# Performance work log

Hardware: AMD Instinct MI355X
Metric: run time of the kernel (lower is better)

Reference implementation:

```python
import jax, jax.numpy as jnp
import numpy as np

N, E, D = 50000, 800000, 128      # nodes, edges, input feature dim
H, HEADS, C = 128, 8, 64          # hidden units, attention heads, classes
HEAD_DIM = H // HEADS
NEG_SLOPE = 0.2


def segment_softmax(scores, seg, num_segments):
    # scores: [E, heads]; softmax over edges sharing the same destination node
    m = jax.ops.segment_max(scores, seg, num_segments=num_segments)
    ex = jnp.exp(scores - m[seg])
    s = jax.ops.segment_sum(ex, seg, num_segments=num_segments)
    return ex / (s[seg] + 1e-9)


def gcn_layer(x, src, dst, W, b):
    # mean-aggregate neighbor features along edges, then linear transform
    agg = jax.ops.segment_sum(x[src], dst, num_segments=N)          # [N, d]
    deg = jax.ops.segment_sum(jnp.ones((E,), x.dtype), dst, num_segments=N)
    agg = agg / jnp.maximum(deg, 1.0)[:, None]
    return agg @ W + b


def gat_layer(x, src, dst, Wg, a_src, a_dst, bg):
    h = (x @ Wg).reshape(N, HEADS, HEAD_DIM)                        # [N, heads, hd]
    e_s = jnp.einsum('nhd,hd->nh', h, a_src)                        # [N, heads]
    e_d = jnp.einsum('nhd,hd->nh', h, a_dst)
    scores = jax.nn.leaky_relu(e_s[src] + e_d[dst], NEG_SLOPE)      # [E, heads]
    alpha = segment_softmax(scores, dst, N)                         # [E, heads]
    msg = h[src] * alpha[:, :, None]                                # [E, heads, hd]
    out = jax.ops.segment_sum(msg, dst, num_segments=N).reshape(N, H)
    return out + bg


def setup_inputs() -> dict:
    key = jax.random.key(0)
    ks = jax.random.split(key, 12)
    s = lambda fan: 1.0 / np.sqrt(fan)
    return {
        'node_features': jax.random.normal(ks[0], (N, D), jnp.float32),
        'edge_index': jax.random.randint(ks[1], (2, E), 0, N, jnp.int32),
        'W1': jax.random.normal(ks[2], (D, H), jnp.float32) * s(D),
        'b1': jnp.zeros((H,), jnp.float32),
        'W2': jax.random.normal(ks[3], (H, H), jnp.float32) * s(H),
        'b2': jnp.zeros((H,), jnp.float32),
        'Wg': jax.random.normal(ks[4], (D, H), jnp.float32) * s(D),
        'bg': jnp.zeros((H,), jnp.float32),
        'a_src': jax.random.normal(ks[5], (HEADS, HEAD_DIM), jnp.float32) * s(HEAD_DIM),
        'a_dst': jax.random.normal(ks[6], (HEADS, HEAD_DIM), jnp.float32) * s(HEAD_DIM),
        'Wcls': jax.random.normal(ks[7], (H, C), jnp.float32) * s(H),
        'bcls': jnp.zeros((C,), jnp.float32),
        'Wl': jax.random.normal(ks[8], (H, 1), jnp.float32) * s(H),
        'bl': jnp.zeros((1,), jnp.float32),
    }


def reference(node_features, edge_index, W1, b1, W2, b2, Wg, bg, a_src, a_dst, Wcls, bcls, Wl, bl):
    src, dst = edge_index[0], edge_index[1]
    x = jax.nn.relu(gcn_layer(node_features, src, dst, W1, b1))
    x = jax.nn.relu(gcn_layer(x, src, dst, W2, b2))
    node_classification_output = jax.nn.softmax(x @ Wcls + bcls, axis=-1)  # [N, C]
    x_gat = jax.nn.relu(gat_layer(node_features, src, dst, Wg, a_src, a_dst, bg))
    link_prediction_output = jax.nn.sigmoid(x_gat @ Wl + bl)               # [N, 1]
    return (node_classification_output, link_prediction_output)
```

## Files before the change

### kernel.cpp

```cpp
#include <hip/hip_runtime.h>
#include <math.h>

#define DIM      128
#define HEADS    8
#define NCLS     64
#define NEG_SLOPE 0.2f
#define NPB32    32
#define NPB64    64
#define APAD     132
#define KT       32
#define CAP      48

typedef unsigned int uint32;

__device__ __forceinline__ uint32 pack_bf162(float a, float b) {
    uint32 ua = __float_as_uint(a); ua += 0x7fffu + ((ua >> 16) & 1u);
    uint32 ub = __float_as_uint(b); ub += 0x7fffu + ((ub >> 16) & 1u);
    return (ua >> 16) | (ub & 0xffff0000u);
}
__device__ __forceinline__ float2 unpack_bf162(uint32 u) {
    return make_float2(__uint_as_float(u << 16), __uint_as_float(u & 0xffff0000u));
}

__global__ __launch_bounds__(256, 4)
void proj1_fill(const float* __restrict__ x, const float* __restrict__ Wg,
                const float* __restrict__ a_src, const float* __restrict__ a_dst,
                uint32* __restrict__ zb, float* __restrict__ e_s,
                float* __restrict__ e_d, int N,
                const int* __restrict__ src, const int* __restrict__ dst,
                int* __restrict__ cursor, unsigned short* __restrict__ ell,
                int E, int nProj) {
    __shared__ float A[NPB64 * APAD];
    int tid = threadIdx.x;
    int bid = blockIdx.x;
    int p = bid / 5;
    bool isProj = ((bid % 5) == 0) && (p < nProj);

    if (!isProj) {
        int projBefore = min((bid + 4) / 5, nProj);
        int e = (bid - projBefore) * 256 + tid;
        if (e < E) {
            int d = dst[e];
            int pos = atomicAdd(&cursor[d], 1);
            if (pos < CAP) ell[(size_t)d * CAP + pos] = (unsigned short)src[e];
        }
        return;
    }

    int n0 = p * NPB64;
    for (int idx = tid; idx < NPB64 * 32; idx += 256) {
        int nl = idx >> 5, qq = idx & 31;
        int n = n0 + nl;
        float4 v = (n < N) ? ((const float4*)x)[(size_t)n * 32 + qq]
                           : make_float4(0.f, 0.f, 0.f, 0.f);
        *(float4*)&A[nl * APAD + qq * 4] = v;
    }
    __syncthreads();

    for (int idx = tid; idx < NPB64 * 16; idx += 256) {
        int nl = idx >> 4, u4 = idx & 15;
        int n = n0 + nl;
        if (n < N) {
            float4 va = *(float4*)&A[nl * APAD + u4 * 8];
            float4 vb = *(float4*)&A[nl * APAD + u4 * 8 + 4];
            uint4 o;
            o.x = pack_bf162(va.x, va.y); o.y = pack_bf162(va.z, va.w);
            o.z = pack_bf162(vb.x, vb.y); o.w = pack_bf162(vb.z, vb.w);
            *(uint4*)(zb + (size_t)n * 128 + u4 * 4) = o;
        }
    }

    int fg = tid & 15, ng = tid >> 4;
    int nb = ng * 4;
    const float* W = Wg + (size_t)fg * 8;
    float acc[4][8];
#pragma unroll
    for (int r = 0; r < 4; ++r)
#pragma unroll
        for (int c = 0; c < 8; ++c) acc[r][c] = 0.f;

#pragma unroll 4
    for (int k = 0; k < DIM; ++k) {
        float wv[8];
        *(float4*)&wv[0] = *(const float4*)(W + (size_t)k * DIM);
        *(float4*)&wv[4] = *(const float4*)(W + (size_t)k * DIM + 4);
#pragma unroll
        for (int r = 0; r < 4; ++r) {
            float a = A[(nb + r) * APAD + k];
#pragma unroll
            for (int c = 0; c < 8; ++c) acc[r][c] = fmaf(a, wv[c], acc[r][c]);
        }
    }
#pragma unroll
    for (int r = 0; r < 4; ++r) {
        int n = n0 + nb + r;
        if (n < N) {
            uint32 o[4];
#pragma unroll
            for (int c = 0; c < 4; ++c) o[c] = pack_bf162(acc[r][2 * c], acc[r][2 * c + 1]);
            *(uint4*)(zb + (size_t)n * 128 + 64 + fg * 4) = *(uint4*)o;
        }
    }
    int head = fg >> 1, sub = (fg & 1) * 8;
    float as[8], ad[8];
#pragma unroll
    for (int j = 0; j < 8; ++j) {
        as[j] = a_src[head * 16 + sub + j];
        ad[j] = a_dst[head * 16 + sub + j];
    }
#pragma unroll
    for (int r = 0; r < 4; ++r) {
        int n = n0 + nb + r;
        float ps = 0.f, pd = 0.f;
#pragma unroll
        for (int c = 0; c < 8; ++c) {
            ps = fmaf(acc[r][c], as[c], ps);
            pd = fmaf(acc[r][c], ad[c], pd);
        }
        ps += __shfl_xor(ps, 1);
        pd += __shfl_xor(pd, 1);
        if (n < N && !(fg & 1)) {
            e_s[n * HEADS + head] = ps;
            e_d[n * HEADS + head] = pd;
        }
    }
}

__global__ __launch_bounds__(256, 8)
void mega1(const uint32* __restrict__ zb, const int* __restrict__ cursor,
           const unsigned short* __restrict__ ell, const float* __restrict__ e_s,
           const float* __restrict__ e_d, const float* __restrict__ bg,
           const float* __restrict__ Wl, const float* __restrict__ bl,
           uint32* __restrict__ mxb, float* __restrict__ out_link, int N) {
    int wave = threadIdx.x >> 6, lane = threadIdx.x & 63;
    int n = blockIdx.x * 4 + wave;
    if (n >= N) return;
    int eoff = lane >> 5, q = lane & 31;
    bool isH = q >= 16;
    int head = (max(q, 16) - 16) >> 1;
    float edl = e_d[n * HEADS + head];
    const uint4* zrow = (const uint4*)zb;
    size_t base = (size_t)n * CAP;
    int len = min(cursor[n], CAP);
    float acc[8];
#pragma unroll
    for (int j = 0; j < 8; ++j) acc[j] = 0.f;
    float den = 0.f;
    int it = 0;
    for (; it + 8 <= len; it += 8) {
        int s[4];
#pragma unroll
        for (int k = 0; k < 4; ++k) s[k] = ell[base + it + 2 * k + eoff];
        float es[4]; uint4 u[4];
#pragma unroll
        for (int k = 0; k < 4; ++k) {
            es[k] = e_s[s[k] * HEADS + head];
            u[k]  = zrow[(size_t)s[k] * 32 + q];
        }
#pragma unroll
        for (int k = 0; k < 4; ++k) {
            float sc = es[k] + edl;
            sc = (sc > 0.f) ? sc : NEG_SLOPE * sc;
            float ex = __expf(sc);
            den += ex;
            float w = isH ? ex : 1.f;
            float2 v0 = unpack_bf162(u[k].x), v1 = unpack_bf162(u[k].y);
            float2 v2 = unpack_bf162(u[k].z), v3 = unpack_bf162(u[k].w);
            acc[0] = fmaf(v0.x, w, acc[0]); acc[1] = fmaf(v0.y, w, acc[1]);
            acc[2] = fmaf(v1.x, w, acc[2]); acc[3] = fmaf(v1.y, w, acc[3]);
            acc[4] = fmaf(v2.x, w, acc[4]); acc[5] = fmaf(v2.y, w, acc[5]);
            acc[6] = fmaf(v3.x, w, acc[6]); acc[7] = fmaf(v3.y, w, acc[7]);
        }
    }
    for (; it < len; it += 2) {
        int e = it + eoff;
        bool valid = e < len;
        int s = ell[base + (valid ? e : it)];
        float sc = e_s[s * HEADS + head] + edl;
        sc = (sc > 0.f) ? sc : NEG_SLOPE * sc;
        float ex = __expf(sc);
        uint4 u = zrow[(size_t)s * 32 + q];
        den += valid ? ex : 0.f;
        float w = valid ? (isH ? ex : 1.f) : 0.f;
        float2 v0 = unpack_bf162(u.x), v1 = unpack_bf162(u.y);
        float2 v2 = unpack_bf162(u.z), v3 = unpack_bf162(u.w);
        acc[0] = fmaf(v0.x, w, acc[0]); acc[1] = fmaf(v0.y, w, acc[1]);
        acc[2] = fmaf(v1.x, w, acc[2]); acc[3] = fmaf(v1.y, w, acc[3]);
        acc[4] = fmaf(v2.x, w, acc[4]); acc[5] = fmaf(v2.y, w, acc[5]);
        acc[6] = fmaf(v3.x, w, acc[6]); acc[7] = fmaf(v3.y, w, acc[7]);
    }
#pragma unroll
    for (int j = 0; j < 8; ++j) acc[j] += __shfl_xor(acc[j], 32);
    den += __shfl_xor(den, 32);

    if (!isH && eoff == 0) {
        float inv = 1.f / fmaxf((float)len, 1.f);
        uint4 o;
        o.x = pack_bf162(acc[0] * inv, acc[1] * inv);
        o.y = pack_bf162(acc[2] * inv, acc[3] * inv);
        o.z = pack_bf162(acc[4] * inv, acc[5] * inv);
        o.w = pack_bf162(acc[6] * inv, acc[7] * inv);
        ((uint4*)(mxb + (size_t)n * 64))[q] = o;
    }
    float p = 0.f;
    if (isH && eoff == 0) {
        float inva = 1.f / (den + 1e-9f);
        int hq = q - 16;
        float4 ga = ((const float4*)bg)[2 * hq];
        float4 gb = ((const float4*)bg)[2 * hq + 1];
        float4 wa = ((const float4*)Wl)[2 * hq];
        float4 wb = ((const float4*)Wl)[2 * hq + 1];
        p = fmaf(fmaxf(acc[0] * inva + ga.x, 0.f), wa.x, p);
        p = fmaf(fmaxf(acc[1] * inva + ga.y, 0.f), wa.y, p);
        p = fmaf(fmaxf(acc[2] * inva + ga.z, 0.f), wa.z, p);
        p = fmaf(fmaxf(acc[3] * inva + ga.w, 0.f), wa.w, p);
        p = fmaf(fmaxf(acc[4] * inva + gb.x, 0.f), wb.x, p);
        p = fmaf(fmaxf(acc[5] * inva + gb.y, 0.f), wb.y, p);
        p = fmaf(fmaxf(acc[6] * inva + gb.z, 0.f), wb.z, p);
        p = fmaf(fmaxf(acc[7] * inva + gb.w, 0.f), wb.w, p);
    }
#pragma unroll
    for (int off = 1; off < 64; off <<= 1) p += __shfl_xor(p, off);
    if (lane == 0) out_link[n] = 1.f / (1.f + expf(-(p + bl[0])));
}

__global__ __launch_bounds__(256, 3)
void proj12(const uint32* __restrict__ mxb, const float* __restrict__ W1,
            const float* __restrict__ b1, const float* __restrict__ W2,
            uint32* __restrict__ y2b, int N) {
    __shared__ float A[NPB64 * APAD];
    __shared__ float Wt[KT * DIM];
    int n0 = blockIdx.x * NPB64;
    int tid = threadIdx.x;
    for (int idx = tid; idx < NPB64 * 64; idx += 256) {
        int nl = idx >> 6, q = idx & 63;
        int n = n0 + nl;
        float2 v = (n < N) ? unpack_bf162(mxb[(size_t)n * 64 + q]) : make_float2(0.f, 0.f);
        A[nl * APAD + 2 * q]     = v.x;
        A[nl * APAD + 2 * q + 1] = v.y;
    }

    int fg = tid & 15, ng = tid >> 4;
    int nb = ng * 4;
    float acc[4][8];
#pragma unroll
    for (int r = 0; r < 4; ++r)
#pragma unroll
        for (int c = 0; c < 8; ++c) acc[r][c] = 0.f;

    for (int kt = 0; kt < DIM; kt += KT) {
        __syncthreads();
        for (int idx = tid; idx < KT * 32; idx += 256) {
            int kk = idx >> 5, c4 = idx & 31;
            *(float4*)&Wt[kk * DIM + c4 * 4] =
                *(const float4*)(W1 + (size_t)(kt + kk) * DIM + c4 * 4);
        }
        __syncthreads();
#pragma unroll 4
        for (int kk = 0; kk < KT; ++kk) {
            float wv[8];
            *(float4*)&wv[0] = *(float4*)&Wt[kk * DIM + fg * 8];
            *(float4*)&wv[4] = *(float4*)&Wt[kk * DIM + fg * 8 + 4];
            int k = kt + kk;
#pragma unroll
            for (int r = 0; r < 4; ++r) {
                float a = A[(nb + r) * APAD + k];
#pragma unroll
                for (int c = 0; c < 8; ++c) acc[r][c] = fmaf(a, wv[c], acc[r][c]);
            }
        }
    }

    float bv[8];
    *(float4*)&bv[0] = ((const float4*)b1)[fg * 2];
    *(float4*)&bv[4] = ((const float4*)b1)[fg * 2 + 1];
    __syncthreads();
#pragma unroll
    for (int r = 0; r < 4; ++r) {
        *(float4*)&A[(nb + r) * APAD + fg * 8] =
            make_float4(fmaxf(acc[r][0] + bv[0], 0.f), fmaxf(acc[r][1] + bv[1], 0.f),
                        fmaxf(acc[r][2] + bv[2], 0.f), fmaxf(acc[r][3] + bv[3], 0.f));
        *(float4*)&A[(nb + r) * APAD + fg * 8 + 4] =
            make_float4(fmaxf(acc[r][4] + bv[4], 0.f), fmaxf(acc[r][5] + bv[5], 0.f),
                        fmaxf(acc[r][6] + bv[6], 0.f), fmaxf(acc[r][7] + bv[7], 0.f));
#pragma unroll
        for (int c = 0; c < 8; ++c) acc[r][c] = 0.f;
    }

    for (int kt = 0; kt < DIM; kt += KT) {
        __syncthreads();
        for (int idx = tid; idx < KT * 32; idx += 256) {
            int kk = idx >> 5, c4 = idx & 31;
            *(float4*)&Wt[kk * DIM + c4 * 4] =
                *(const float4*)(W2 + (size_t)(kt + kk) * DIM + c4 * 4);
        }
        __syncthreads();
#pragma unroll 4
        for (int kk = 0; kk < KT; ++kk) {
            float wv[8];
            *(float4*)&wv[0] = *(float4*)&Wt[kk * DIM + fg * 8];
            *(float4*)&wv[4] = *(float4*)&Wt[kk * DIM + fg * 8 + 4];
            int k = kt + kk;
#pragma unroll
            for (int r = 0; r < 4; ++r) {
                float a = A[(nb + r) * APAD + k];
#pragma unroll
                for (int c = 0; c < 8; ++c) acc[r][c] = fmaf(a, wv[c], acc[r][c]);
            }
        }
    }

#pragma unroll
    for (int r = 0; r < 4; ++r) {
        int n = n0 + nb + r;
        if (n < N) {
            uint32 o[4];
#pragma unroll
            for (int c = 0; c < 4; ++c) o[c] = pack_bf162(acc[r][2 * c], acc[r][2 * c + 1]);
            *(uint4*)(y2b + (size_t)n * 64 + fg * 4) = *(uint4*)o;
        }
    }
}

__global__ __launch_bounds__(256, 8)
void mega2(const uint32* __restrict__ y2b, const int* __restrict__ cursor,
           const unsigned short* __restrict__ ell, const float* __restrict__ b2,
           const float* __restrict__ Wcls, const float* __restrict__ bcls,
           float* __restrict__ out_cls, int N) {
    __shared__ float A[NPB32 * APAD];
    int tid = threadIdx.x;
    int wave = tid >> 6, lane = tid & 63;
    int eoff = lane >> 4, q = lane & 15;
    int n0 = blockIdx.x * NPB32;
    const uint4* yrow = (const uint4*)y2b;

    for (int i = 0; i < 8; ++i) {
        int nl = wave * 8 + i;
        int n = n0 + nl;
        int len = (n < N) ? min(cursor[n], CAP) : 0;
        size_t base = (size_t)n * CAP;
        float acc[8];
#pragma unroll
        for (int j = 0; j < 8; ++j) acc[j] = 0.f;
        int it = 0;
        for (; it + 16 <= len; it += 16) {
            int s[4];
#pragma unroll
            for (int k = 0; k < 4; ++k) s[k] = ell[base + it + 4 * k + eoff];
            uint4 u[4];
#pragma unroll
            for (int k = 0; k < 4; ++k) u[k] = yrow[(size_t)s[k] * 16 + q];
#pragma unroll
            for (int k = 0; k < 4; ++k) {
                float2 v0 = unpack_bf162(u[k].x), v1 = unpack_bf162(u[k].y);
                float2 v2 = unpack_bf162(u[k].z), v3 = unpack_bf162(u[k].w);
                acc[0] += v0.x; acc[1] += v0.y; acc[2] += v1.x; acc[3] += v1.y;
                acc[4] += v2.x; acc[5] += v2.y; acc[6] += v3.x; acc[7] += v3.y;
            }
        }
        for (; it + 8 <= len; it += 8) {
            int s[2];
#pragma unroll
            for (int k = 0; k < 2; ++k) s[k] = ell[base + it + 4 * k + eoff];
            uint4 u[2];
#pragma unroll
            for (int k = 0; k < 2; ++k) u[k] = yrow[(size_t)s[k] * 16 + q];
#pragma unroll
            for (int k = 0; k < 2; ++k) {
                float2 v0 = unpack_bf162(u[k].x), v1 = unpack_bf162(u[k].y);
                float2 v2 = unpack_bf162(u[k].z), v3 = unpack_bf162(u[k].w);
                acc[0] += v0.x; acc[1] += v0.y; acc[2] += v1.x; acc[3] += v1.y;
                acc[4] += v2.x; acc[5] += v2.y; acc[6] += v3.x; acc[7] += v3.y;
            }
        }
        for (; it < len; it += 4) {
            int e = it + eoff;
            bool valid = e < len;
            int s = ell[base + (valid ? e : it)];
            uint4 u = yrow[(size_t)s * 16 + q];
            float w = valid ? 1.f : 0.f;
            float2 v0 = unpack_bf162(u.x), v1 = unpack_bf162(u.y);
            float2 v2 = unpack_bf162(u.z), v3 = unpack_bf162(u.w);
            acc[0] = fmaf(v0.x, w, acc[0]); acc[1] = fmaf(v0.y, w, acc[1]);
            acc[2] = fmaf(v1.x, w, acc[2]); acc[3] = fmaf(v1.y, w, acc[3]);
            acc[4] = fmaf(v2.x, w, acc[4]); acc[5] = fmaf(v2.y, w, acc[5]);
            acc[6] = fmaf(v3.x, w, acc[6]); acc[7] = fmaf(v3.y, w, acc[7]);
        }
#pragma unroll
        for (int j = 0; j < 8; ++j) {
            acc[j] += __shfl_xor(acc[j], 16);
            acc[j] += __shfl_xor(acc[j], 32);
        }
        if (eoff == 0) {
            float inv = 1.f / fmaxf((float)len, 1.f);
            float4 ba = ((const float4*)b2)[2 * q];
            float4 bb = ((const float4*)b2)[2 * q + 1];
            float4 xa, xb;
            xa.x = fmaxf(acc[0] * inv + ba.x, 0.f); xa.y = fmaxf(acc[1] * inv + ba.y, 0.f);
            xa.z = fmaxf(acc[2] * inv + ba.z, 0.f); xa.w = fmaxf(acc[3] * inv + ba.w, 0.f);
            xb.x = fmaxf(acc[4] * inv + bb.x, 0.f); xb.y = fmaxf(acc[5] * inv + bb.y, 0.f);
            xb.z = fmaxf(acc[6] * inv + bb.z, 0.f); xb.w = fmaxf(acc[7] * inv + bb.w, 0.f);
            *(float4*)&A[nl * APAD + 8 * q]     = xa;
            *(float4*)&A[nl * APAD + 8 * q + 4] = xb;
        }
    }
    __syncthreads();

    int fg = tid & 15, ng = tid >> 4;
    int nm = ng * 2, c0 = fg * 4;
    float accC[2][4];
#pragma unroll
    for (int r = 0; r < 2; ++r)
#pragma unroll
        for (int c = 0; c < 4; ++c) accC[r][c] = 0.f;
    const float4* Wc4 = (const float4*)Wcls;
#pragma unroll 4
    for (int k = 0; k < DIM; ++k) {
        float a0 = A[nm * APAD + k];
        float a1 = A[(nm + 1) * APAD + k];
        float wv[4];
        *(float4*)&wv[0] = Wc4[k * 16 + fg];
#pragma unroll
        for (int c = 0; c < 4; ++c) {
            accC[0][c] = fmaf(a0, wv[c], accC[0][c]);
            accC[1][c] = fmaf(a1, wv[c], accC[1][c]);
        }
    }
    float4 bv = ((const float4*)bcls)[fg];
    float cb[4] = {bv.x, bv.y, bv.z, bv.w};
#pragma unroll
    for (int r = 0; r < 2; ++r) {
        int n = n0 + nm + r;
        float l[4];
        float m = -1e30f;
#pragma unroll
        for (int c = 0; c < 4; ++c) { l[c] = accC[r][c] + cb[c]; m = fmaxf(m, l[c]); }
        for (int off = 1; off < 16; off <<= 1) m = fmaxf(m, __shfl_xor(m, off));
        float s = 0.f;
#pragma unroll
        for (int c = 0; c < 4; ++c) { l[c] = expf(l[c] - m); s += l[c]; }
        for (int off = 1; off < 16; off <<= 1) s += __shfl_xor(s, off);
        float invs = 1.f / s;
        if (n < N) {
            float4 o = {l[0] * invs, l[1] * invs, l[2] * invs, l[3] * invs};
            *(float4*)(out_cls + (size_t)n * NCLS + c0) = o;
        }
    }
}

extern "C" void kernel_launch(void* const* d_in, const int* in_sizes, int n_in,
                              void* d_out, int out_size, void* d_ws, size_t ws_size,
                              hipStream_t stream) {
    const float* xin   = (const float*)d_in[0];
    const int*   eidx  = (const int*)  d_in[1];
    const float* W1    = (const float*)d_in[2];
    const float* b1    = (const float*)d_in[3];
    const float* W2    = (const float*)d_in[4];
    const float* b2    = (const float*)d_in[5];
    const float* Wg    = (const float*)d_in[6];
    const float* bg    = (const float*)d_in[7];
    const float* a_src = (const float*)d_in[8];
    const float* a_dst = (const float*)d_in[9];
    const float* Wcls  = (const float*)d_in[10];
    const float* bcls  = (const float*)d_in[11];
    const float* Wl    = (const float*)d_in[12];
    const float* bl    = (const float*)d_in[13];

    const int N = in_sizes[0] / DIM;
    const int E = in_sizes[1] / 2;
    const int* src = eidx;
    const int* dst = eidx + E;

    char* ws = (char*)d_ws;
    size_t off = 0;
    int* cursor = (int*)(ws + off);
    off = (off + (size_t)N * sizeof(int) + 15) & ~(size_t)15;
    unsigned short* ell = (unsigned short*)(ws + off);
    off = (off + (size_t)N * CAP * sizeof(unsigned short) + 15) & ~(size_t)15;
    float* e_s = (float*)(ws + off);
    off = (off + (size_t)N * HEADS * sizeof(float) + 15) & ~(size_t)15;
    float* e_d = (float*)(ws + off);
    off = (off + (size_t)N * HEADS * sizeof(float) + 15) & ~(size_t)15;
    uint32* zb = (uint32*)(ws + off);
    off = (off + (size_t)N * 128 * sizeof(uint32) + 15) & ~(size_t)15;
    uint32* mxb = (uint32*)(ws + off);
    uint32* y2b = zb;

    float* out_cls  = (float*)d_out;
    float* out_link = out_cls + (size_t)N * NCLS;

    int blkE   = (E + 255) / 256;
    int blkN4  = (N + 3) / 4;
    int blkN32 = (N + NPB32 - 1) / NPB32;
    int blkN64 = (N + NPB64 - 1) / NPB64;

    hipMemsetAsync(cursor, 0, (size_t)N * sizeof(int), stream);
    proj1_fill<<<blkN64 + blkE, 256, 0, stream>>>(xin, Wg, a_src, a_dst,
                                                  zb, e_s, e_d, N,
                                                  src, dst, cursor, ell, E, blkN64);

    mega1<<<blkN4, 256, 0, stream>>>(zb, cursor, ell, e_s, e_d,
                                     bg, Wl, bl, mxb, out_link, N);

    proj12<<<blkN64, 256, 0, stream>>>(mxb, W1, b1, W2, y2b, N);

    mega2<<<blkN32, 256, 0, stream>>>(y2b, cursor, ell, b2,
                                      Wcls, bcls, out_cls, N);
}
```

Baseline: 368.0 us.

## Drop LDS staging in projection, batch four edges per fill thread, interleave roles

The fused projection/ELL-fill kernel no longer stages the 64-node input tile in shared memory. The GEMM reads x rows directly from global memory through per-row pointers, which frees LDS and raises the occupancy hint from 4 to 6 waves. Fill blocks now handle 1024 edges each, with four loads issued before the atomics, and projection and fill blocks alternate one-to-one in the grid. The aim is more overlap and less LDS pressure, at the cost of repeated global or L1 reads of x inside the k-loop, since each row is now read by 16 threads.

Result: slower. 434.3 us (+18.0%).

```diff
diff --git a/kernel.cpp b/kernel.cpp
--- a/kernel.cpp
+++ b/kernel.cpp
@@ -22,7 +22,7 @@
     return make_float2(__uint_as_float(u << 16), __uint_as_float(u & 0xffff0000u));
 }
 
-__global__ __launch_bounds__(256, 4)
+__global__ __launch_bounds__(256, 6)
 void proj1_fill(const float* __restrict__ x, const float* __restrict__ Wg,
                 const float* __restrict__ a_src, const float* __restrict__ a_dst,
                 uint32* __restrict__ zb, float* __restrict__ e_s,
@@ -30,39 +30,44 @@
                 const int* __restrict__ src, const int* __restrict__ dst,
                 int* __restrict__ cursor, unsigned short* __restrict__ ell,
                 int E, int nProj) {
-    __shared__ float A[NPB64 * APAD];
     int tid = threadIdx.x;
     int bid = blockIdx.x;
-    int p = bid / 5;
-    bool isProj = ((bid % 5) == 0) && (p < nProj);
-
-    if (!isProj) {
-        int projBefore = min((bid + 4) / 5, nProj);
-        int e = (bid - projBefore) * 256 + tid;
-        if (e < E) {
-            int d = dst[e];
-            int pos = atomicAdd(&cursor[d], 1);
-            if (pos < CAP) ell[(size_t)d * CAP + pos] = (unsigned short)src[e];
+    int nFill = gridDim.x - nProj;
+    int mn = min(nProj, nFill);
+    int role, idx;
+    if (bid < 2 * mn) { role = bid & 1; idx = bid >> 1; }
+    else { idx = bid - mn; role = (nProj > nFill) ? 0 : 1; }
+
+    if (role == 1) {
+        int e0 = idx * 1024 + tid;
+        int dd[4], ss[4];
+        bool v[4];
+#pragma unroll
+        for (int j = 0; j < 4; ++j) {
+            int e = e0 + j * 256;
+            v[j] = e < E;
+            int ec = min(e, E - 1);
+            dd[j] = dst[ec];
+            ss[j] = src[ec];
+        }
+#pragma unroll
+        for (int j = 0; j < 4; ++j) {
+            if (v[j]) {
+                int pos = atomicAdd(&cursor[dd[j]], 1);
+                if (pos < CAP) ell[(size_t)dd[j] * CAP + pos] = (unsigned short)ss[j];
+            }
         }
         return;
     }
 
-    int n0 = p * NPB64;
-    for (int idx = tid; idx < NPB64 * 32; idx += 256) {
-        int nl = idx >> 5, qq = idx & 31;
-        int n = n0 + nl;
-        float4 v = (n < N) ? ((const float4*)x)[(size_t)n * 32 + qq]
-                           : make_float4(0.f, 0.f, 0.f, 0.f);
-        *(float4*)&A[nl * APAD + qq * 4] = v;
-    }
-    __syncthreads();
-
-    for (int idx = tid; idx < NPB64 * 16; idx += 256) {
-        int nl = idx >> 4, u4 = idx & 15;
+    int n0 = idx * NPB64;
+
+    for (int t = tid; t < NPB64 * 16; t += 256) {
+        int nl = t >> 4, u4 = t & 15;
         int n = n0 + nl;
         if (n < N) {
-            float4 va = *(float4*)&A[nl * APAD + u4 * 8];
-            float4 vb = *(float4*)&A[nl * APAD + u4 * 8 + 4];
+            float4 va = ((const float4*)x)[(size_t)n * 32 + 2 * u4];
+            float4 vb = ((const float4*)x)[(size_t)n * 32 + 2 * u4 + 1];
             uint4 o;
             o.x = pack_bf162(va.x, va.y); o.y = pack_bf162(va.z, va.w);
             o.z = pack_bf162(vb.x, vb.y); o.w = pack_bf162(vb.z, vb.w);
@@ -72,6 +77,10 @@
 
     int fg = tid & 15, ng = tid >> 4;
     int nb = ng * 4;
+    const float* rp[4];
+#pragma unroll
+    for (int r = 0; r < 4; ++r)
+        rp[r] = x + (size_t)min(n0 + nb + r, N - 1) * DIM;
     const float* W = Wg + (size_t)fg * 8;
     float acc[4][8];
 #pragma unroll
@@ -86,7 +95,7 @@
         *(float4*)&wv[4] = *(const float4*)(W + (size_t)k * DIM + 4);
 #pragma unroll
         for (int r = 0; r < 4; ++r) {
-            float a = A[(nb + r) * APAD + k];
+            float a = rp[r][k];
 #pragma unroll
             for (int c = 0; c < 8; ++c) acc[r][c] = fmaf(a, wv[c], acc[r][c]);
         }
@@ -489,15 +498,15 @@
     float* out_cls  = (float*)d_out;
     float* out_link = out_cls + (size_t)N * NCLS;
 
-    int blkE   = (E + 255) / 256;
+    int blkE4  = (E + 1023) / 1024;
     int blkN4  = (N + 3) / 4;
     int blkN32 = (N + NPB32 - 1) / NPB32;
     int blkN64 = (N + NPB64 - 1) / NPB64;
 
     hipMemsetAsync(cursor, 0, (size_t)N * sizeof(int), stream);
-    proj1_fill<<<blkN64 + blkE, 256, 0, stream>>>(xin, Wg, a_src, a_dst,
-                                                  zb, e_s, e_d, N,
-                                                  src, dst, cursor, ell, E, blkN64);
+    proj1_fill<<<blkN64 + blkE4, 256, 0, stream>>>(xin, Wg, a_src, a_dst,
+                                                   zb, e_s, e_d, N,
+                                                   src, dst, cursor, ell, E, blkN64);
 
     mega1<<<blkN4, 256, 0, stream>>>(zb, cursor, ell, e_s, e_d,
                                      bg, Wl, bl, mxb, out_link, N);
```
